# Kernel tuning notes

Measured on AMD Instinct MI355X. Metric: run time of the kernel, lower is better.

The kernel has to match this reference:

```python
import jax, jax.numpy as jnp
import numpy as np

# --- static configuration (matches init_kwargs / input_specs) ---
B, QB, D, NH, HD = 4, 512, 256, 8, 32   # batch, queries/batch, d_model, heads, head_dim
HALF = HD // 2                            # rotation pairs per head
L = 4                                     # n_levels
SIZES = [3, 5, 7, 9]                      # neighborhood size per level
K = sum(s * s for s in SIZES)             # 164 keys per query
SHAPES = np.array([[8, 8], [16, 16], [32, 32], [64, 64]], dtype=np.int32)
HMAX = 64                                 # finest-level spatial extent
LN_EPS = 1e-5
ROPE_THETA = 10.0


def make_rope_freqs():
    # Grouped-frequency ND RoPE: spatial dims (i, j) in freq group 0 (theta=10),
    # level dim in group 1 (theta = rope_theta/100 = 0.1). HALF slots split:
    # group0 -> HALF/2 (HALF/4 per spatial dim), group1 -> HALF/2.
    n_sp = HALF // 4   # 4 slots for i, 4 for j
    n_lv = HALF // 2   # 8 slots for level
    f = np.zeros((3, HALF), np.float32)
    f_sp = ROPE_THETA ** (-np.arange(n_sp, dtype=np.float32) / n_sp)
    f_lv = (ROPE_THETA / 100.0) ** (-np.arange(n_lv, dtype=np.float32) / n_lv)
    f[0, 0:n_sp] = f_sp
    f[1, n_sp:2 * n_sp] = f_sp
    f[2, 2 * n_sp:] = f_lv
    return jnp.asarray(np.tile(f[None], (NH, 1, 1)))  # [NH, 3, HALF]


def neighborhood_indices(qpos, shapes):
    # qpos: [N,4] float (b, i, j, level); queries live at the finest level so
    # (i, j) are full-scale coords. Returns (b,i,j,l) int indices [N,K,4] and
    # full-scale key positions (i_full, j_full, level) [N,K,3].
    N = qpos.shape[0]
    b = qpos[:, 0].astype(jnp.int32)
    q_ij = qpos[:, 1:3]
    shapes_f = shapes.astype(jnp.float32)
    scal = shapes_f / shapes_f[-1]  # [L,2]: H_l / H_finest
    idx_parts, pos_parts = [], []
    for m, size in enumerate(SIZES):
        center = jnp.floor(q_ij * scal[m]).astype(jnp.int32)  # [N,2] at level m
        r = jnp.arange(size, dtype=jnp.int32) - (size - 1) // 2
        off = jnp.stack(jnp.meshgrid(r, r, indexing='ij'), -1).reshape(-1, 2)
        nb = center[:, None, :] + off[None]                    # [N, s*s, 2]
        lev_i = jnp.full((N, size * size, 1), m, jnp.int32)
        idx_parts.append(jnp.concatenate([nb, lev_i], -1))
        pos_parts.append(jnp.concatenate(
            [nb.astype(jnp.float32) / scal[m],                 # back to full scale
             jnp.full((N, size * size, 1), float(m))], -1))
    ijl = jnp.concatenate(idx_parts, 1)       # [N,K,3]
    key_pos = jnp.concatenate(pos_parts, 1)   # [N,K,3]
    bijl = jnp.concatenate([jnp.broadcast_to(b[:, None, None], (N, K, 1)), ijl], -1)
    return bijl, key_pos


def gather_values(fmap, bijl, shapes):
    # fmap: dense stand-in for the sparse COO pyramid, [B, HMAX, HMAX, L, D];
    # level l only occupies the top-left [H_l, W_l] block -> out-of-range keys
    # are "unspecified" (value 0, masked out of the softmax).
    b, i, j, l = bijl[..., 0], bijl[..., 1], bijl[..., 2], bijl[..., 3]
    hw = shapes[l]  # [N,K,2]
    valid = (i >= 0) & (i < hw[..., 0]) & (j >= 0) & (j < hw[..., 1])
    ic = jnp.clip(i, 0, HMAX - 1)
    jc = jnp.clip(j, 0, HMAX - 1)
    val = fmap[b, ic, jc, l]  # [N,K,D]
    return val * valid[..., None], valid


def layer_norm(x, g, b_):
    mu = x.mean(-1, keepdims=True)
    var = ((x - mu) ** 2).mean(-1, keepdims=True)
    return (x - mu) * jax.lax.rsqrt(var + LN_EPS) * g + b_


def apply_rope(x, pos, freqs):
    # x: [..., NH, HD], pos: [..., 3], freqs: [NH, 3, HALF]
    ang = jnp.einsum('...p,hpf->...hf', pos, freqs)
    c, s = jnp.cos(ang), jnp.sin(ang)
    xr = x.reshape(x.shape[:-1] + (HALF, 2))
    x1, x2 = xr[..., 0], xr[..., 1]
    return jnp.stack([x1 * c - x2 * s, x1 * s + x2 * c], -1).reshape(x.shape)


def setup_inputs() -> dict:
    key = jax.random.key(0)
    ks = jax.random.split(key, 8)
    N = B * QB
    q_ij = jax.random.uniform(ks[0], (N, 2), minval=0.5, maxval=float(HMAX) - 0.5)
    batch = jnp.repeat(jnp.arange(B, dtype=jnp.float32), QB)
    lev = jnp.full((N, 1), float(L - 1))  # all queries at the finest level
    query_positions_bijl = jnp.concatenate([batch[:, None], q_ij, lev], -1)
    sc = D ** -0.5
    return {
        'query': jax.random.normal(ks[1], (N, D), jnp.float32),
        'query_positions_bijl': query_positions_bijl,
        'query_batch_offsets': jnp.arange(B + 1, dtype=jnp.int32) * QB,
        'stacked_feature_maps': jax.random.normal(ks[2], (B, HMAX, HMAX, L, D), jnp.float32),
        'level_spatial_shapes': jnp.asarray(SHAPES),
        'ln_gamma': jnp.ones((D,), jnp.float32),
        'ln_beta': jnp.zeros((D,), jnp.float32),
        'Wq': jax.random.normal(ks[3], (D, D), jnp.float32) * sc,
        'Wkv': jax.random.normal(ks[4], (D, 2 * D), jnp.float32) * sc,
        'Wout': jax.random.normal(ks[5], (D, D), jnp.float32) * sc,
        'rope_freqs': make_rope_freqs(),
    }


def reference(query, query_positions_bijl, query_batch_offsets, stacked_feature_maps,
              level_spatial_shapes, ln_gamma, ln_beta, Wq, Wkv, Wout, rope_freqs):
    N = query.shape[0]
    bijl, key_pos = neighborhood_indices(query_positions_bijl, level_spatial_shapes)
    value, specified = gather_values(stacked_feature_maps, bijl, level_spatial_shapes)
    residual = query
    qn = layer_norm(query, ln_gamma, ln_beta)  # norm_first
    q = qn @ Wq                                # [N, D]
    kv = value @ Wkv                           # [N, K, 2D]
    k, v = jnp.split(kv, 2, axis=-1)
    q = apply_rope(q.reshape(B, QB, NH, HD),
                   query_positions_bijl[:, 1:].reshape(B, QB, 3), rope_freqs)
    k = apply_rope(k.reshape(B, QB, K, NH, HD),
                   key_pos.reshape(B, QB, K, 3), rope_freqs)
    v = v.reshape(B, QB, K, NH, HD)
    # NOTE: original module applies no 1/sqrt(head_dim) scaling -- kept faithful.
    scores = jnp.einsum('bqhd,bqkhd->bhqk', q, k)
    mask = specified.reshape(B, QB, K)[:, None]  # [B,1,QB,K]
    scores = jnp.where(mask, scores, -jnp.inf)
    w = jax.nn.softmax(scores, axis=-1)
    x = jnp.einsum('bhqk,bqkhd->bqhd', w, v)
    x = x.reshape(N, D) @ Wout
    return x + residual
```

## Files before the change

### kernel.cpp

```cpp
#include <hip/hip_runtime.h>
#include <math.h>

#define NQ    2048
#define Dd    256
#define NHh   8
#define HDd   32
#define KK    164
#define KP    192
#define PPB   5440
#define M_TOT 21760
#define TWO_D 512

using bf16x8  = __attribute__((ext_vector_type(8))) short;
using f32x4   = __attribute__((ext_vector_type(4))) float;
using ushort8 = __attribute__((ext_vector_type(8))) unsigned short;

__device__ __forceinline__ unsigned short bf16_rne(float x) {
    unsigned u = __float_as_uint(x);
    return (unsigned short)((u + 0x7fffu + ((u >> 16) & 1u)) >> 16);
}
__device__ __forceinline__ float bf2f(unsigned short h) {
    return __uint_as_float((unsigned)h << 16);
}

__device__ __forceinline__ void gload_lds16(const void* g, void* s) {
    __builtin_amdgcn_global_load_lds(
        (const __attribute__((address_space(1))) void*)g,
        (__attribute__((address_space(3))) void*)s, 16, 0, 0);
}

__device__ __forceinline__ void row_geom(int r, int& l, int& S, int& base, int& lg, int& inv) {
    if      (r < 64)   { l = 0; S = 8;  base = 0;    lg = 3; inv = 8; }
    else if (r < 320)  { l = 1; S = 16; base = 64;   lg = 4; inv = 4; }
    else if (r < 1344) { l = 2; S = 32; base = 320;  lg = 5; inv = 2; }
    else               { l = 3; S = 64; base = 1344; lg = 6; inv = 1; }
}

__global__ __launch_bounds__(256) void gather_split(const float* __restrict__ fmap,
                                                    unsigned short* __restrict__ Ahi,
                                                    unsigned short* __restrict__ Alo) {
    int gid = blockIdx.x * 256 + threadIdx.x;
    int m = gid >> 6, c4 = (gid & 63) << 2;
    int b = m / PPB, r = m - b * PPB;
    int l, S, base, lg, inv;
    row_geom(r, l, S, base, lg, inv);
    int idx = r - base;
    int i = idx >> lg, j = idx & (S - 1);
    size_t rowOff = ((size_t)((b * 64 + i) * 64 + j)) * 1024 + l * 256;
    const float4 v = *(const float4*)(fmap + rowOff + c4);
    ushort4 hi, lo;
    hi.x = bf16_rne(v.x); lo.x = bf16_rne(v.x - __uint_as_float((unsigned)hi.x << 16));
    hi.y = bf16_rne(v.y); lo.y = bf16_rne(v.y - __uint_as_float((unsigned)hi.y << 16));
    hi.z = bf16_rne(v.z); lo.z = bf16_rne(v.z - __uint_as_float((unsigned)hi.z << 16));
    hi.w = bf16_rne(v.w); lo.w = bf16_rne(v.w - __uint_as_float((unsigned)hi.w << 16));
    *(ushort4*)(Ahi + (size_t)m * 256 + c4) = hi;
    *(ushort4*)(Alo + (size_t)m * 256 + c4) = lo;
}

__global__ __launch_bounds__(256) void splitw_t(const float* __restrict__ W,
                                                unsigned short* __restrict__ Bthi,
                                                unsigned short* __restrict__ Btlo,
                                                int N) {
    int gid = blockIdx.x * 256 + threadIdx.x;
    int k = gid & 255, n = gid >> 8;
    float x = W[k * N + n];
    unsigned short h = bf16_rne(x);
    unsigned short lo = bf16_rne(x - __uint_as_float((unsigned)h << 16));
    Bthi[n * 256 + k] = h;
    Btlo[n * 256 + k] = lo;
}

__global__ __launch_bounds__(256) void kv_gemm_mfma(const unsigned short* __restrict__ Ahi,
                                                    const unsigned short* __restrict__ Alo,
                                                    const unsigned short* __restrict__ Bthi,
                                                    const unsigned short* __restrict__ Btlo,
                                                    unsigned short* __restrict__ kv16) {
    __shared__ __align__(16) short As[2][128 * 32];
    __shared__ __align__(16) short Bs[2][128 * 32];

    const int t  = threadIdx.x;
    const int w  = t >> 6, l = t & 63;
    const int wr = w >> 1, wc = w & 1;
    const int bm = blockIdx.x * 128, n0 = blockIdx.y * 128;
    const int lr = l & 15, ks = l >> 4;
    const int ksw8 = ((ks ^ ((lr >> 1) & 3)) << 3);

    f32x4 acc[4][4];
#pragma unroll
    for (int i = 0; i < 4; i++)
#pragma unroll
        for (int j = 0; j < 4; j++) { f32x4 z = {0.f,0.f,0.f,0.f}; acc[i][j] = z; }

    const int srow = l >> 2, sslot = l & 3;
    const int gs = sslot ^ ((srow >> 1) & 3);

    auto stage = [&](int kt, int buf) {
        int seg = kt >> 3;
        const unsigned short* Aseg = (seg < 2) ? Ahi : Alo;
        const unsigned short* Bseg = (seg == 1) ? Btlo : Bthi;
        size_t k0b = (size_t)((kt & 7) << 6);
#pragma unroll
        for (int i = 0; i < 2; i++) {
            int rb = w * 32 + i * 16;
            int m  = rb + srow;
            gload_lds16((const char*)Aseg + (((size_t)(bm + m)) << 9) + k0b + (gs << 4),
                        (void*)&As[buf][rb * 32]);
            gload_lds16((const char*)Bseg + (((size_t)(n0 + m)) << 9) + k0b + (gs << 4),
                        (void*)&Bs[buf][rb * 32]);
        }
    };

    stage(0, 0);
    __syncthreads();

    for (int kt = 0; kt < 24; kt++) {
        int cur = kt & 1;
        if (kt < 23) stage(kt + 1, cur ^ 1);

        bf16x8 afr[4], bfr[4];
#pragma unroll
        for (int f = 0; f < 4; f++) {
            int m = wr * 64 + f * 16 + lr;
            afr[f] = *(const bf16x8*)&As[cur][m * 32 + ksw8];
            int n = wc * 64 + f * 16 + lr;
            bfr[f] = *(const bf16x8*)&Bs[cur][n * 32 + ksw8];
        }
#pragma unroll
        for (int i = 0; i < 4; i++)
#pragma unroll
            for (int j = 0; j < 4; j++)
                acc[i][j] = __builtin_amdgcn_mfma_f32_16x16x32_bf16(afr[i], bfr[j],
                                                                    acc[i][j], 0, 0, 0);
        __syncthreads();
    }

#pragma unroll
    for (int i = 0; i < 4; i++) {
        int mg = bm + wr * 64 + i * 16 + ks * 4;
#pragma unroll
        for (int j = 0; j < 4; j++) {
            int ng = n0 + wc * 64 + j * 16 + lr;
#pragma unroll
            for (int r = 0; r < 4; r++) {
                float self = acc[i][j][r];
                float part = __shfl_xor(self, 1);
                if (!(lr & 1)) {
                    unsigned word = (unsigned)bf16_rne(self)
                                  | ((unsigned)bf16_rne(part) << 16);
                    *(unsigned*)(kv16 + (size_t)(mg + r) * TWO_D + ng) = word;
                }
            }
        }
    }
}

template<bool RESID>
__global__ __launch_bounds__(256) void proj_gemm(const unsigned short* __restrict__ Ahi,
                                                 const unsigned short* __restrict__ Alo,
                                                 const unsigned short* __restrict__ Bthi,
                                                 const unsigned short* __restrict__ Btlo,
                                                 float* __restrict__ C,
                                                 const float* __restrict__ resid) {
    __shared__ __align__(16) short As[2][128 * 32];
    __shared__ __align__(16) short Bs[2][64 * 32];

    const int t  = threadIdx.x;
    const int w  = t >> 6, l = t & 63;
    const int bm = blockIdx.x * 128, n0 = blockIdx.y * 64;
    const int lr = l & 15, ks = l >> 4;
    const int ksw8 = ((ks ^ ((lr >> 1) & 3)) << 3);

    f32x4 acc[2][4];
#pragma unroll
    for (int i = 0; i < 2; i++)
#pragma unroll
        for (int j = 0; j < 4; j++) { f32x4 z = {0.f,0.f,0.f,0.f}; acc[i][j] = z; }

    const int srow = l >> 2, sslot = l & 3;
    const int gs = sslot ^ ((srow >> 1) & 3);

    auto stage = [&](int kt, int buf) {
        int seg = kt >> 3;
        const unsigned short* Aseg = (seg < 2) ? Ahi : Alo;
        const unsigned short* Bseg = (seg == 1) ? Btlo : Bthi;
        size_t k0b = (size_t)((kt & 7) << 6);
#pragma unroll
        for (int i = 0; i < 2; i++) {
            int rb = w * 32 + i * 16;
            int m  = rb + srow;
            gload_lds16((const char*)Aseg + (((size_t)(bm + m)) << 9) + k0b + (gs << 4),
                        (void*)&As[buf][rb * 32]);
        }
        {
            int rb = w * 16;
            int m  = rb + srow;
            gload_lds16((const char*)Bseg + (((size_t)(n0 + m)) << 9) + k0b + (gs << 4),
                        (void*)&Bs[buf][rb * 32]);
        }
    };

    stage(0, 0);
    __syncthreads();

    for (int kt = 0; kt < 24; kt++) {
        int cur = kt & 1;
        if (kt < 23) stage(kt + 1, cur ^ 1);

        bf16x8 afr[2], bfr[4];
#pragma unroll
        for (int f = 0; f < 2; f++) {
            int m = w * 32 + f * 16 + lr;
            afr[f] = *(const bf16x8*)&As[cur][m * 32 + ksw8];
        }
#pragma unroll
        for (int j = 0; j < 4; j++) {
            int n = j * 16 + lr;
            bfr[j] = *(const bf16x8*)&Bs[cur][n * 32 + ksw8];
        }
#pragma unroll
        for (int i = 0; i < 2; i++)
#pragma unroll
            for (int j = 0; j < 4; j++)
                acc[i][j] = __builtin_amdgcn_mfma_f32_16x16x32_bf16(afr[i], bfr[j],
                                                                    acc[i][j], 0, 0, 0);
        __syncthreads();
    }

#pragma unroll
    for (int i = 0; i < 2; i++) {
        int mg = bm + w * 32 + i * 16 + ks * 4;
#pragma unroll
        for (int j = 0; j < 4; j++) {
            int ng = n0 + j * 16 + lr;
#pragma unroll
            for (int r = 0; r < 4; r++) {
                float v = acc[i][j][r];
                if (RESID) v += resid[(size_t)(mg + r) * 256 + ng];
                C[(size_t)(mg + r) * 256 + ng] = v;
            }
        }
    }
}

__global__ __launch_bounds__(256) void rope_k(unsigned short* __restrict__ kv16,
                                              const float* __restrict__ freqs) {
    int gid = blockIdx.x * 256 + threadIdx.x;
    int m = gid >> 7;
    int p = gid & 127;
    int f = p & 15;

    int b = m / PPB;
    int r = m - b * PPB;
    int l, S, base, lg, inv;
    row_geom(r, l, S, base, lg, inv);
    int idx = r - base;
    int i = idx >> lg;
    int j = idx & (S - 1);

    float px = (float)(i * inv), py = (float)(j * inv), pl = (float)l;
    float ang = px * freqs[f] + py * freqs[16 + f] + pl * freqs[32 + f];
    float c = cosf(ang), s = sinf(ang);

    unsigned* kp = (unsigned*)kv16 + (size_t)m * 256 + p;
    unsigned v = *kp;
    float x1 = bf2f((unsigned short)(v & 0xffff));
    float x2 = bf2f((unsigned short)(v >> 16));
    float y1 = x1 * c - x2 * s;
    float y2 = x1 * s + x2 * c;
    *kp = (unsigned)bf16_rne(y1) | ((unsigned)bf16_rne(y2) << 16);
}

__global__ __launch_bounds__(256) void ln_split(const float* __restrict__ query,
                                                const float* __restrict__ gamma,
                                                const float* __restrict__ beta,
                                                unsigned short* __restrict__ Xhi,
                                                unsigned short* __restrict__ Xlo) {
    __shared__ float red[4];
    const int q = blockIdx.x, t = threadIdx.x, wid = t >> 6;

    float x = query[q * Dd + t];
    float s = x;
#pragma unroll
    for (int mK = 32; mK >= 1; mK >>= 1) s += __shfl_xor(s, mK);
    if ((t & 63) == 0) red[wid] = s;
    __syncthreads();
    float mu = (red[0] + red[1] + red[2] + red[3]) * (1.0f / 256.0f);
    float dx = x - mu;
    float s2 = dx * dx;
#pragma unroll
    for (int mK = 32; mK >= 1; mK >>= 1) s2 += __shfl_xor(s2, mK);
    __syncthreads();
    if ((t & 63) == 0) red[wid] = s2;
    __syncthreads();
    float var = (red[0] + red[1] + red[2] + red[3]) * (1.0f / 256.0f);
    float v = dx * rsqrtf(var + 1e-5f) * gamma[t] + beta[t];
    unsigned short hi = bf16_rne(v);
    Xhi[q * Dd + t] = hi;
    Xlo[q * Dd + t] = bf16_rne(v - __uint_as_float((unsigned)hi << 16));
}

__global__ __launch_bounds__(256) void attn_core(const float* __restrict__ qr,
                                                 const float* __restrict__ qpos,
                                                 const unsigned short* __restrict__ kv16,
                                                 const float* __restrict__ freqs,
                                                 unsigned short* __restrict__ Phi,
                                                 unsigned short* __restrict__ Plo) {
    __shared__ __align__(16) float qsh[Dd];
    __shared__ float sL[NHh * KP];
    __shared__ int   kidx[KP];
    __shared__ float attnP[8][Dd];
    __shared__ float invS[NHh];

    const int q = ((blockIdx.x & 7) << 8) | (blockIdx.x >> 3);
    const int t = threadIdx.x;
    const int h = t >> 5, lane = t & 31;

    float qx = qpos[q * 4 + 1];
    float qy = qpos[q * 4 + 2];
    int   bb = (int)qpos[q * 4 + 0];

    {
        float x = qr[q * Dd + t];
        int f = (t & 31) >> 1;
        float ang = qx * freqs[f] + qy * freqs[16 + f] + 3.0f * freqs[32 + f];
        float c = cosf(ang), sn = sinf(ang);
        float partner = __shfl_xor(x, 1);
        qsh[t] = (!(t & 1)) ? (x * c - partner * sn) : (partner * sn + x * c);
    }

    if (t < KP) {
        int k = t;
        int kv = -1;
        if (k < KK) {
            int S, base, off, sz, half, lg;
            if      (k < 9)  { S = 8;  base = 0;    off = k;      sz = 3; half = 1; lg = 3; }
            else if (k < 34) { S = 16; base = 64;   off = k - 9;  sz = 5; half = 2; lg = 4; }
            else if (k < 83) { S = 32; base = 320;  off = k - 34; sz = 7; half = 3; lg = 5; }
            else             { S = 64; base = 1344; off = k - 83; sz = 9; half = 4; lg = 6; }
            int di = off / sz - half;
            int dj = off % sz - half;
            float scal = (float)S * (1.0f / 64.0f);
            int ci = (int)floorf(qx * scal);
            int cj = (int)floorf(qy * scal);
            int i = ci + di, j = cj + dj;
            bool valid = (i >= 0) & (i < S) & (j >= 0) & (j < S);
            kv = valid ? (bb * PPB + base + (i << lg) + j) : -1;
        }
        kidx[t] = kv;
    }
    __syncthreads();

    float qreg[32];
#pragma unroll
    for (int i = 0; i < 32; i++) qreg[i] = qsh[h * HDd + i];

#pragma unroll
    for (int ct = 0; ct < 6; ++ct) {
        int k = ct * 32 + lane;
        int ki = kidx[k];
        int kr = ki < 0 ? 0 : ki;
        const ushort8* kp = (const ushort8*)(kv16 + (size_t)kr * TWO_D + h * HDd);
        float c0 = 0.f, c1 = 0.f;
#pragma unroll
        for (int s4 = 0; s4 < 4; s4++) {
            ushort8 kvv = kp[s4];
            float* cc = (s4 & 1) ? &c1 : &c0;
#pragma unroll
            for (int e = 0; e < 8; e++)
                *cc = fmaf(qreg[s4 * 8 + e], bf2f(kvv[e]), *cc);
        }
        sL[h * KP + k] = (ki >= 0) ? (c0 + c1) : -INFINITY;
    }
    __syncthreads();

    float mx = -INFINITY;
#pragma unroll
    for (int ct = 0; ct < 6; ++ct) mx = fmaxf(mx, sL[h * KP + ct * 32 + lane]);
#pragma unroll
    for (int mK = 16; mK >= 1; mK >>= 1) mx = fmaxf(mx, __shfl_xor(mx, mK));
    float se = 0.f;
#pragma unroll
    for (int ct = 0; ct < 6; ++ct) {
        int k = ct * 32 + lane;
        float e = __expf(sL[h * KP + k] - mx);
        sL[h * KP + k] = e;
        se += e;
    }
#pragma unroll
    for (int mK = 16; mK >= 1; mK >>= 1) se += __shfl_xor(se, mK);
    if (lane == 0) invS[h] = 1.0f / se;
    __syncthreads();

    {
        const int rep  = t >> 6;
        const int half = (t >> 5) & 1;
        const int l5   = t & 31;
        const int hh   = l5 >> 2;
        const int oct  = l5 & 3;
        float a[8];
#pragma unroll
        for (int e = 0; e < 8; e++) a[e] = 0.f;
        const unsigned short* vbase = kv16 + Dd + hh * HDd + oct * 8;
#pragma unroll 4
        for (int it = 0; it < 24; it++) {
            int k = rep * 48 + it * 2 + half;
            float w0 = sL[hh * KP + k];
            int kr = kidx[k]; kr = kr < 0 ? 0 : kr;
            ushort8 vv = *(const ushort8*)(vbase + (size_t)kr * TWO_D);
#pragma unroll
            for (int e = 0; e < 8; e++) a[e] = fmaf(w0, bf2f(vv[e]), a[e]);
        }
        float* dst = &attnP[t >> 5][hh * HDd + oct * 8];
#pragma unroll
        for (int e = 0; e < 8; e++) dst[e] = a[e];
    }
    __syncthreads();

    float val = 0.f;
#pragma unroll
    for (int s = 0; s < 8; s++) val += attnP[s][t];
    val *= invS[h];
    unsigned short hi = bf16_rne(val);
    Phi[q * Dd + t] = hi;
    Plo[q * Dd + t] = bf16_rne(val - __uint_as_float((unsigned)hi << 16));
}

#define BMf 128
#define BNf 128
#define KTf 16

__global__ __launch_bounds__(256) void kv_gemm(const float* __restrict__ fmap,
                                               const float* __restrict__ Wkv,
                                               float* __restrict__ kvws) {
    __shared__ float Asf[KTf][BMf + 4];
    __shared__ float Bsf[KTf][BNf + 4];
    __shared__ int   rowOff[BMf];

    const int t  = threadIdx.x;
    const int bm = blockIdx.x * BMf;
    const int n0 = blockIdx.y * BNf;

    if (t < BMf) {
        int m = bm + t;
        int b = m / PPB;
        int r = m - b * PPB;
        int l, S, base, lg, inv;
        row_geom(r, l, S, base, lg, inv);
        int idx = r - base;
        int i = idx >> lg;
        int j = idx & (S - 1);
        rowOff[t] = ((b * 64 + i) * 64 + j) * 1024 + l * 256;
    }
    __syncthreads();

    const int tx = t & 15, ty = t >> 4;
    float acc[8][8];
#pragma unroll
    for (int i = 0; i < 8; i++)
#pragma unroll
        for (int j = 0; j < 8; j++) acc[i][j] = 0.f;

    for (int k0 = 0; k0 < Dd; k0 += KTf) {
#pragma unroll
        for (int s = 0; s < 2; s++) {
            int task = t + s * 256;
            int row  = task >> 2;
            int k4   = (task & 3) * 4;
            const float4 v = *(const float4*)(fmap + rowOff[row] + k0 + k4);
            Asf[k4 + 0][row] = v.x;
            Asf[k4 + 1][row] = v.y;
            Asf[k4 + 2][row] = v.z;
            Asf[k4 + 3][row] = v.w;
        }
#pragma unroll
        for (int s = 0; s < 2; s++) {
            int task = t + s * 256;
            int kk   = task >> 5;
            int c4   = (task & 31) * 4;
            *(float4*)(&Bsf[kk][c4]) = *(const float4*)(Wkv + (k0 + kk) * TWO_D + n0 + c4);
        }
        __syncthreads();
#pragma unroll
        for (int kk = 0; kk < KTf; kk++) {
            float a[8], bb[8];
#pragma unroll
            for (int i = 0; i < 8; i++) a[i]  = Asf[kk][ty * 8 + i];
#pragma unroll
            for (int j = 0; j < 8; j++) bb[j] = Bsf[kk][tx * 8 + j];
#pragma unroll
            for (int i = 0; i < 8; i++)
#pragma unroll
                for (int j = 0; j < 8; j++)
                    acc[i][j] = fmaf(a[i], bb[j], acc[i][j]);
        }
        __syncthreads();
    }

#pragma unroll
    for (int i = 0; i < 8; i++) {
        int m = bm + ty * 8 + i;
        float* dst = kvws + (size_t)m * TWO_D + n0 + tx * 8;
#pragma unroll
        for (int j = 0; j < 8; j += 4) {
            *(float4*)(dst + j) = make_float4(acc[i][j], acc[i][j + 1],
                                              acc[i][j + 2], acc[i][j + 3]);
        }
    }
}

__global__ __launch_bounds__(256) void rope_k_f32(float* __restrict__ kvws,
                                                  const float* __restrict__ freqs) {
    int gid = blockIdx.x * 256 + threadIdx.x;
    int m = gid >> 7;
    int p = gid & 127;
    int f = p & 15;
    int b = m / PPB;
    int r = m - b * PPB;
    int l, S, base, lg, inv;
    row_geom(r, l, S, base, lg, inv);
    int idx = r - base;
    int i = idx >> lg;
    int j = idx & (S - 1);
    float px = (float)(i * inv), py = (float)(j * inv), pl = (float)l;
    float ang = px * freqs[f] + py * freqs[16 + f] + pl * freqs[32 + f];
    float c = cosf(ang), s = sinf(ang);
    float2* kp = (float2*)kvws + (size_t)m * 256 + p;
    float2 v = *kp;
    *kp = make_float2(v.x * c - v.y * s, v.x * s + v.y * c);
}

__global__ __launch_bounds__(256) void attn_fused(const float* __restrict__ query,
                                                  const float* __restrict__ qpos,
                                                  const float* __restrict__ Wq,
                                                  const float* __restrict__ Wout,
                                                  const float* __restrict__ gamma,
                                                  const float* __restrict__ beta,
                                                  const float* __restrict__ freqs,
                                                  const float* __restrict__ kvws,
                                                  float* __restrict__ out) {
    __shared__ float qn[Dd];
    __shared__ __align__(16) float qsh[Dd];
    __shared__ float sL[NHh * KK];
    __shared__ int   kidx[KK];
    __shared__ float attnL[Dd];
    __shared__ float red[4];
    __shared__ float invS[NHh];

    const int q = blockIdx.x;
    const int t = threadIdx.x;
    const int wid = t >> 6;
    const int h = t >> 5, lane = t & 31;

    float x = query[q * Dd + t];
    float s = x;
#pragma unroll
    for (int mK = 32; mK >= 1; mK >>= 1) s += __shfl_xor(s, mK);
    if ((t & 63) == 0) red[wid] = s;
    __syncthreads();
    float mu = (red[0] + red[1] + red[2] + red[3]) * (1.0f / 256.0f);
    float dx = x - mu;
    float s2 = dx * dx;
#pragma unroll
    for (int mK = 32; mK >= 1; mK >>= 1) s2 += __shfl_xor(s2, mK);
    __syncthreads();
    if ((t & 63) == 0) red[wid] = s2;
    __syncthreads();
    float var = (red[0] + red[1] + red[2] + red[3]) * (1.0f / 256.0f);
    float rs = rsqrtf(var + 1e-5f);
    qn[t] = dx * rs * gamma[t] + beta[t];
    __syncthreads();

    float a0 = 0.f, a1 = 0.f, a2 = 0.f, a3 = 0.f;
#pragma unroll 8
    for (int d = 0; d < Dd; d += 4) {
        a0 = fmaf(qn[d + 0], Wq[(d + 0) * Dd + t], a0);
        a1 = fmaf(qn[d + 1], Wq[(d + 1) * Dd + t], a1);
        a2 = fmaf(qn[d + 2], Wq[(d + 2) * Dd + t], a2);
        a3 = fmaf(qn[d + 3], Wq[(d + 3) * Dd + t], a3);
    }
    float acc = (a0 + a1) + (a2 + a3);

    float qx = qpos[q * 4 + 1];
    float qy = qpos[q * 4 + 2];
    int   bb = (int)qpos[q * 4 + 0];
    {
        int f = (t & 31) >> 1;
        float ang = qx * freqs[f] + qy * freqs[16 + f] + 3.0f * freqs[32 + f];
        float c = cosf(ang), sn = sinf(ang);
        float partner = __shfl_xor(acc, 1);
        bool ev = !(t & 1);
        acc = ev ? (acc * c - partner * sn) : (partner * sn + acc * c);
    }
    qsh[t] = acc;

    if (t < KK) {
        int k = t;
        int S, base, off, sz, half, lg;
        if      (k < 9)  { S = 8;  base = 0;    off = k;      sz = 3; half = 1; lg = 3; }
        else if (k < 34) { S = 16; base = 64;   off = k - 9;  sz = 5; half = 2; lg = 4; }
        else if (k < 83) { S = 32; base = 320;  off = k - 34; sz = 7; half = 3; lg = 5; }
        else             { S = 64; base = 1344; off = k - 83; sz = 9; half = 4; lg = 6; }
        int di = off / sz - half;
        int dj = off % sz - half;
        float scal = (float)S * (1.0f / 64.0f);
        int ci = (int)floorf(qx * scal);
        int cj = (int)floorf(qy * scal);
        int i = ci + di, j = cj + dj;
        bool valid = (i >= 0) & (i < S) & (j >= 0) & (j < S);
        kidx[t] = valid ? (bb * PPB + base + (i << lg) + j) : -1;
    }
    __syncthreads();

    float4 qv[8];
    {
        const float4* qp = (const float4*)(qsh + h * HDd);
#pragma unroll
        for (int i = 0; i < 8; i++) qv[i] = qp[i];
    }
#pragma unroll
    for (int ct = 0; ct < 6; ++ct) {
        int k = ct * 32 + lane;
        if (k >= KK) break;
        int ki = kidx[k];
        int kr = ki < 0 ? 0 : ki;
        const float4* kp = (const float4*)(kvws + (size_t)kr * TWO_D + h * HDd);
        float c0 = 0.f, c1 = 0.f;
#pragma unroll
        for (int i = 0; i < 8; i += 2) {
            float4 k0v = kp[i], k1v = kp[i + 1];
            c0 = fmaf(qv[i].x, k0v.x, c0); c0 = fmaf(qv[i].y, k0v.y, c0);
            c0 = fmaf(qv[i].z, k0v.z, c0); c0 = fmaf(qv[i].w, k0v.w, c0);
            c1 = fmaf(qv[i + 1].x, k1v.x, c1); c1 = fmaf(qv[i + 1].y, k1v.y, c1);
            c1 = fmaf(qv[i + 1].z, k1v.z, c1); c1 = fmaf(qv[i + 1].w, k1v.w, c1);
        }
        sL[h * KK + k] = (ki >= 0) ? (c0 + c1) : -INFINITY;
    }
    __syncthreads();

    float mx = -INFINITY;
    for (int k = lane; k < KK; k += 32) mx = fmaxf(mx, sL[h * KK + k]);
#pragma unroll
    for (int mK = 16; mK >= 1; mK >>= 1) mx = fmaxf(mx, __shfl_xor(mx, mK));
    float se = 0.f;
    for (int k = lane; k < KK; k += 32) {
        float e = expf(sL[h * KK + k] - mx);
        sL[h * KK + k] = e;
        se += e;
    }
#pragma unroll
    for (int mK = 16; mK >= 1; mK >>= 1) se += __shfl_xor(se, mK);
    if (lane == 0) invS[h] = 1.0f / se;
    __syncthreads();

    float p0 = 0.f, p1 = 0.f, p2 = 0.f, p3 = 0.f;
#pragma unroll 4
    for (int k = 0; k < 164; k += 4) {
        int ki0 = kidx[k],     kr0 = ki0 < 0 ? 0 : ki0;
        int ki1 = kidx[k + 1], kr1 = ki1 < 0 ? 0 : ki1;
        int ki2 = kidx[k + 2], kr2 = ki2 < 0 ? 0 : ki2;
        int ki3 = kidx[k + 3], kr3 = ki3 < 0 ? 0 : ki3;
        p0 = fmaf(sL[h * KK + k],     kvws[(size_t)kr0 * TWO_D + Dd + t], p0);
        p1 = fmaf(sL[h * KK + k + 1], kvws[(size_t)kr1 * TWO_D + Dd + t], p1);
        p2 = fmaf(sL[h * KK + k + 2], kvws[(size_t)kr2 * TWO_D + Dd + t], p2);
        p3 = fmaf(sL[h * KK + k + 3], kvws[(size_t)kr3 * TWO_D + Dd + t], p3);
    }
    attnL[t] = ((p0 + p1) + (p2 + p3)) * invS[h];
    __syncthreads();

    float o0 = query[q * Dd + t], o1 = 0.f, o2 = 0.f, o3 = 0.f;
#pragma unroll 8
    for (int d = 0; d < Dd; d += 4) {
        o0 = fmaf(attnL[d + 0], Wout[(d + 0) * Dd + t], o0);
        o1 = fmaf(attnL[d + 1], Wout[(d + 1) * Dd + t], o1);
        o2 = fmaf(attnL[d + 2], Wout[(d + 2) * Dd + t], o2);
        o3 = fmaf(attnL[d + 3], Wout[(d + 3) * Dd + t], o3);
    }
    out[q * Dd + t] = (o0 + o1) + (o2 + o3);
}

extern "C" void kernel_launch(void* const* d_in, const int* in_sizes, int n_in,
                              void* d_out, int out_size, void* d_ws, size_t ws_size,
                              hipStream_t stream) {
    const float* query = (const float*)d_in[0];
    const float* qpos  = (const float*)d_in[1];
    const float* fmap  = (const float*)d_in[3];
    const float* gamma = (const float*)d_in[5];
    const float* beta  = (const float*)d_in[6];
    const float* Wq    = (const float*)d_in[7];
    const float* Wkv   = (const float*)d_in[8];
    const float* Wout  = (const float*)d_in[9];
    const float* freqs = (const float*)d_in[10];
    float* out = (float*)d_out;

    const size_t KV_B = (size_t)M_TOT * TWO_D * 4;
    const size_t A_B  = (size_t)M_TOT * Dd * 2;
    const size_t WT_B = (size_t)Dd * TWO_D * 2;
    const size_t need = KV_B + 2 * A_B + 2 * WT_B;

    if (ws_size >= need) {
        char* base = (char*)d_ws;
        unsigned short* kv16   = (unsigned short*)base;
        unsigned short* Ahi    = (unsigned short*)(base + KV_B);
        unsigned short* Alo    = (unsigned short*)(base + KV_B + A_B);
        unsigned short* WkvThi = (unsigned short*)(base + KV_B + 2 * A_B);
        unsigned short* WkvTlo = (unsigned short*)(base + KV_B + 2 * A_B + WT_B);
        unsigned short* Phi    = (unsigned short*)(base + KV_B);
        unsigned short* Plo    = (unsigned short*)(base + KV_B + 1048576);
        float*          qrw    = (float*)        (base + KV_B + 2097152);
        unsigned short* WqThi  = (unsigned short*)(base + KV_B + 4194304);
        unsigned short* WqTlo  = (unsigned short*)(base + KV_B + 4325376);
        unsigned short* WoThi  = (unsigned short*)(base + KV_B + 4456448);
        unsigned short* WoTlo  = (unsigned short*)(base + KV_B + 4587520);

        gather_split<<<dim3((M_TOT * 64) / 256), 256, 0, stream>>>(fmap, Ahi, Alo);
        splitw_t<<<dim3(512), 256, 0, stream>>>(Wkv, WkvThi, WkvTlo, 512);
        kv_gemm_mfma<<<dim3(M_TOT / 128, 4), 256, 0, stream>>>(Ahi, Alo, WkvThi, WkvTlo, kv16);
        rope_k<<<dim3((M_TOT * 128) / 256), 256, 0, stream>>>(kv16, freqs);
        ln_split<<<dim3(NQ), 256, 0, stream>>>(query, gamma, beta, Phi, Plo);
        splitw_t<<<dim3(256), 256, 0, stream>>>(Wq, WqThi, WqTlo, 256);
        splitw_t<<<dim3(256), 256, 0, stream>>>(Wout, WoThi, WoTlo, 256);
        proj_gemm<false><<<dim3(NQ / 128, 4), 256, 0, stream>>>(Phi, Plo, WqThi, WqTlo,
                                                                qrw, nullptr);
        attn_core<<<dim3(NQ), 256, 0, stream>>>(qrw, qpos, kv16, freqs, Phi, Plo);
        proj_gemm<true><<<dim3(NQ / 128, 4), 256, 0, stream>>>(Phi, Plo, WoThi, WoTlo,
                                                               out, query);
    } else {
        float* kvws = (float*)d_ws;
        kv_gemm<<<dim3(M_TOT / BMf, TWO_D / BNf), 256, 0, stream>>>(fmap, Wkv, kvws);
        rope_k_f32<<<dim3((M_TOT * 128) / 256), 256, 0, stream>>>(kvws, freqs);
        attn_fused<<<dim3(NQ), 256, 0, stream>>>(query, qpos, Wq, Wout, gamma, beta,
                                                 freqs, kvws, out);
    }
}
```

Measured before the change: 223.0 us.

## Fuse prep kernels, fold RoPE into KV GEMM epilogue, shrink projection tiles

Merges the gather/split, the three weight-split kernels and the LayerNorm split into one prep launch. The separate K RoPE pass moves into the KV GEMM epilogue, so kv16 is no longer read and rewritten. The grid axes are swapped so column tiles of the same row block run adjacently. The projection GEMMs move to 64x32 tiles, giving more blocks for better occupancy on the small N=2048 problem. This cuts launch overhead and one full pass over the KV buffer, at the cost of extra trig work and branching in the GEMM epilogue.

```diff
diff --git a/kernel.cpp b/kernel.cpp
--- a/kernel.cpp
+++ b/kernel.cpp
@@ -36,44 +36,89 @@
     else               { l = 3; S = 64; base = 1344; lg = 6; inv = 1; }
 }
 
-__global__ __launch_bounds__(256) void gather_split(const float* __restrict__ fmap,
-                                                    unsigned short* __restrict__ Ahi,
-                                                    unsigned short* __restrict__ Alo) {
-    int gid = blockIdx.x * 256 + threadIdx.x;
-    int m = gid >> 6, c4 = (gid & 63) << 2;
-    int b = m / PPB, r = m - b * PPB;
-    int l, S, base, lg, inv;
-    row_geom(r, l, S, base, lg, inv);
-    int idx = r - base;
-    int i = idx >> lg, j = idx & (S - 1);
-    size_t rowOff = ((size_t)((b * 64 + i) * 64 + j)) * 1024 + l * 256;
-    const float4 v = *(const float4*)(fmap + rowOff + c4);
-    ushort4 hi, lo;
-    hi.x = bf16_rne(v.x); lo.x = bf16_rne(v.x - __uint_as_float((unsigned)hi.x << 16));
-    hi.y = bf16_rne(v.y); lo.y = bf16_rne(v.y - __uint_as_float((unsigned)hi.y << 16));
-    hi.z = bf16_rne(v.z); lo.z = bf16_rne(v.z - __uint_as_float((unsigned)hi.z << 16));
-    hi.w = bf16_rne(v.w); lo.w = bf16_rne(v.w - __uint_as_float((unsigned)hi.w << 16));
-    *(ushort4*)(Ahi + (size_t)m * 256 + c4) = hi;
-    *(ushort4*)(Alo + (size_t)m * 256 + c4) = lo;
-}
-
-__global__ __launch_bounds__(256) void splitw_t(const float* __restrict__ W,
-                                                unsigned short* __restrict__ Bthi,
-                                                unsigned short* __restrict__ Btlo,
-                                                int N) {
-    int gid = blockIdx.x * 256 + threadIdx.x;
+__device__ __forceinline__ void split_one(const float* __restrict__ W,
+                                          unsigned short* __restrict__ hi_,
+                                          unsigned short* __restrict__ lo_,
+                                          int N, int gid) {
     int k = gid & 255, n = gid >> 8;
     float x = W[k * N + n];
     unsigned short h = bf16_rne(x);
-    unsigned short lo = bf16_rne(x - __uint_as_float((unsigned)h << 16));
-    Bthi[n * 256 + k] = h;
-    Btlo[n * 256 + k] = lo;
+    hi_[n * 256 + k] = h;
+    lo_[n * 256 + k] = bf16_rne(x - bf2f(h));
+}
+
+__global__ __launch_bounds__(256) void prep(const float* __restrict__ fmap,
+                                            const float* __restrict__ Wkv,
+                                            const float* __restrict__ Wq,
+                                            const float* __restrict__ Wout,
+                                            const float* __restrict__ query,
+                                            const float* __restrict__ gamma,
+                                            const float* __restrict__ beta,
+                                            unsigned short* __restrict__ Ahi,
+                                            unsigned short* __restrict__ Alo,
+                                            unsigned short* __restrict__ WkvThi,
+                                            unsigned short* __restrict__ WkvTlo,
+                                            unsigned short* __restrict__ WqThi,
+                                            unsigned short* __restrict__ WqTlo,
+                                            unsigned short* __restrict__ WoThi,
+                                            unsigned short* __restrict__ WoTlo,
+                                            unsigned short* __restrict__ Xhi,
+                                            unsigned short* __restrict__ Xlo) {
+    __shared__ float red[4];
+    const int bid = blockIdx.x, t = threadIdx.x;
+
+    if (bid < 5440) {
+        int gid = bid * 256 + t;
+        int m = gid >> 6, c4 = (gid & 63) << 2;
+        int b = m / PPB, r = m - b * PPB;
+        int l, S, base, lg, inv;
+        row_geom(r, l, S, base, lg, inv);
+        int idx = r - base;
+        int i = idx >> lg, j = idx & (S - 1);
+        size_t rowOff = ((size_t)((b * 64 + i) * 64 + j)) * 1024 + l * 256;
+        const float4 v = *(const float4*)(fmap + rowOff + c4);
+        ushort4 hi, lo;
+        hi.x = bf16_rne(v.x); lo.x = bf16_rne(v.x - bf2f(hi.x));
+        hi.y = bf16_rne(v.y); lo.y = bf16_rne(v.y - bf2f(hi.y));
+        hi.z = bf16_rne(v.z); lo.z = bf16_rne(v.z - bf2f(hi.z));
+        hi.w = bf16_rne(v.w); lo.w = bf16_rne(v.w - bf2f(hi.w));
+        *(ushort4*)(Ahi + (size_t)m * 256 + c4) = hi;
+        *(ushort4*)(Alo + (size_t)m * 256 + c4) = lo;
+    } else if (bid < 5952) {
+        split_one(Wkv, WkvThi, WkvTlo, 512, (bid - 5440) * 256 + t);
+    } else if (bid < 6208) {
+        split_one(Wq, WqThi, WqTlo, 256, (bid - 5952) * 256 + t);
+    } else if (bid < 6464) {
+        split_one(Wout, WoThi, WoTlo, 256, (bid - 6208) * 256 + t);
+    } else {
+        const int q = bid - 6464, wid = t >> 6;
+        float x = query[q * Dd + t];
+        float s = x;
+#pragma unroll
+        for (int mK = 32; mK >= 1; mK >>= 1) s += __shfl_xor(s, mK);
+        if ((t & 63) == 0) red[wid] = s;
+        __syncthreads();
+        float mu = (red[0] + red[1] + red[2] + red[3]) * (1.0f / 256.0f);
+        float dx = x - mu;
+        float s2 = dx * dx;
+#pragma unroll
+        for (int mK = 32; mK >= 1; mK >>= 1) s2 += __shfl_xor(s2, mK);
+        __syncthreads();
+        if ((t & 63) == 0) red[wid] = s2;
+        __syncthreads();
+        float var = (red[0] + red[1] + red[2] + red[3]) * (1.0f / 256.0f);
+        float v = dx * rsqrtf(var + 1e-5f) * gamma[t] + beta[t];
+        unsigned short hi = bf16_rne(v);
+        Xhi[q * Dd + t] = hi;
+        Xlo[q * Dd + t] = bf16_rne(v - bf2f(hi));
+    }
 }
 
 __global__ __launch_bounds__(256) void kv_gemm_mfma(const unsigned short* __restrict__ Ahi,
                                                     const unsigned short* __restrict__ Alo,
                                                     const unsigned short* __restrict__ Bthi,
                                                     const unsigned short* __restrict__ Btlo,
+                                                    const float* __restrict__ freqs,
                                                     unsigned short* __restrict__ kv16) {
     __shared__ __align__(16) short As[2][128 * 32];
     __shared__ __align__(16) short Bs[2][128 * 32];
@@ -81,9 +126,10 @@
     const int t  = threadIdx.x;
     const int w  = t >> 6, l = t & 63;
     const int wr = w >> 1, wc = w & 1;
-    const int bm = blockIdx.x * 128, n0 = blockIdx.y * 128;
+    const int n0 = blockIdx.x * 128, bm = blockIdx.y * 128;
     const int lr = l & 15, ks = l >> 4;
     const int ksw8 = ((ks ^ ((lr >> 1) & 3)) << 3);
+    const bool doRope = (n0 < 256);
 
     f32x4 acc[4][4];
 #pragma unroll
@@ -138,16 +184,35 @@
     for (int i = 0; i < 4; i++) {
         int mg = bm + wr * 64 + i * 16 + ks * 4;
 #pragma unroll
-        for (int j = 0; j < 4; j++) {
-            int ng = n0 + wc * 64 + j * 16 + lr;
-#pragma unroll
-            for (int r = 0; r < 4; r++) {
+        for (int r = 0; r < 4; r++) {
+            int m = mg + r;
+            float px = 0.f, py = 0.f, pl = 0.f;
+            if (doRope) {
+                int b = m / PPB;
+                int rr = m - b * PPB;
+                int lL, S, base, lg, inv;
+                row_geom(rr, lL, S, base, lg, inv);
+                int idx = rr - base;
+                px = (float)((idx >> lg) * inv);
+                py = (float)((idx & (S - 1)) * inv);
+                pl = (float)lL;
+            }
+#pragma unroll
+            for (int j = 0; j < 4; j++) {
+                int ng = n0 + wc * 64 + j * 16 + lr;
                 float self = acc[i][j][r];
                 float part = __shfl_xor(self, 1);
                 if (!(lr & 1)) {
-                    unsigned word = (unsigned)bf16_rne(self)
-                                  | ((unsigned)bf16_rne(part) << 16);
-                    *(unsigned*)(kv16 + (size_t)(mg + r) * TWO_D + ng) = word;
+                    float y1 = self, y2 = part;
+                    if (doRope) {
+                        int f = (ng & 31) >> 1;
+                        float ang = px * freqs[f] + py * freqs[16 + f] + pl * freqs[32 + f];
+                        float c = cosf(ang), s = sinf(ang);
+                        y1 = self * c - part * s;
+                        y2 = self * s + part * c;
+                    }
+                    unsigned word = (unsigned)bf16_rne(y1) | ((unsigned)bf16_rne(y2) << 16);
+                    *(unsigned*)(kv16 + (size_t)m * TWO_D + ng) = word;
                 }
             }
         }
@@ -161,20 +226,18 @@
                                                  const unsigned short* __restrict__ Btlo,
                                                  float* __restrict__ C,
                                                  const float* __restrict__ resid) {
-    __shared__ __align__(16) short As[2][128 * 32];
-    __shared__ __align__(16) short Bs[2][64 * 32];
+    __shared__ __align__(16) short As[2][64 * 32];
+    __shared__ __align__(16) short Bs[2][32 * 32];
 
     const int t  = threadIdx.x;
     const int w  = t >> 6, l = t & 63;
-    const int bm = blockIdx.x * 128, n0 = blockIdx.y * 64;
+    const int n0 = blockIdx.x * 32, bm = blockIdx.y * 64;
     const int lr = l & 15, ks = l >> 4;
     const int ksw8 = ((ks ^ ((lr >> 1) & 3)) << 3);
 
-    f32x4 acc[2][4];
-#pragma unroll
-    for (int i = 0; i < 2; i++)
-#pragma unroll
-        for (int j = 0; j < 4; j++) { f32x4 z = {0.f,0.f,0.f,0.f}; acc[i][j] = z; }
+    f32x4 acc[2];
+#pragma unroll
+    for (int j = 0; j < 2; j++) { f32x4 z = {0.f,0.f,0.f,0.f}; acc[j] = z; }
 
     const int srow = l >> 2, sslot = l & 3;
     const int gs = sslot ^ ((srow >> 1) & 3);
@@ -184,14 +247,13 @@
         const unsigned short* Aseg = (seg < 2) ? Ahi : Alo;
         const unsigned short* Bseg = (seg == 1) ? Btlo : Bthi;
         size_t k0b = (size_t)((kt & 7) << 6);
-#pragma unroll
-        for (int i = 0; i < 2; i++) {
-            int rb = w * 32 + i * 16;
+        {
+            int rb = w * 16;
             int m  = rb + srow;
             gload_lds16((const char*)Aseg + (((size_t)(bm + m)) << 9) + k0b + (gs << 4),
                         (void*)&As[buf][rb * 32]);
         }
-        {
+        if (w < 2) {
             int rb = w * 16;
             int m  = rb + srow;
             gload_lds16((const char*)Bseg + (((size_t)(n0 + m)) << 9) + k0b + (gs << 4),
@@ -206,97 +268,35 @@
         int cur = kt & 1;
         if (kt < 23) stage(kt + 1, cur ^ 1);
 
-        bf16x8 afr[2], bfr[4];
-#pragma unroll
-        for (int f = 0; f < 2; f++) {
-            int m = w * 32 + f * 16 + lr;
-            afr[f] = *(const bf16x8*)&As[cur][m * 32 + ksw8];
-        }
-#pragma unroll
-        for (int j = 0; j < 4; j++) {
+        bf16x8 afr, bfr[2];
+        {
+            int m = w * 16 + lr;
+            afr = *(const bf16x8*)&As[cur][m * 32 + ksw8];
+        }
+#pragma unroll
+        for (int j = 0; j < 2; j++) {
             int n = j * 16 + lr;
             bfr[j] = *(const bf16x8*)&Bs[cur][n * 32 + ksw8];
         }
 #pragma unroll
-        for (int i = 0; i < 2; i++)
-#pragma unroll
-            for (int j = 0; j < 4; j++)
-                acc[i][j] = __builtin_amdgcn_mfma_f32_16x16x32_bf16(afr[i], bfr[j],
-                                                                    acc[i][j], 0, 0, 0);
+        for (int j = 0; j < 2; j++)
+            acc[j] = __builtin_amdgcn_mfma_f32_16x16x32_bf16(afr, bfr[j], acc[j], 0, 0, 0);
         __syncthreads();
     }
 
-#pragma unroll
-    for (int i = 0; i < 2; i++) {
-        int mg = bm + w * 32 + i * 16 + ks * 4;
-#pragma unroll
-        for (int j = 0; j < 4; j++) {
+    {
+        int mg = bm + w * 16 + ks * 4;
+#pragma unroll
+        for (int j = 0; j < 2; j++) {
             int ng = n0 + j * 16 + lr;
 #pragma unroll
             for (int r = 0; r < 4; r++) {
-                float v = acc[i][j][r];
+                float v = acc[j][r];
                 if (RESID) v += resid[(size_t)(mg + r) * 256 + ng];
                 C[(size_t)(mg + r) * 256 + ng] = v;
             }
         }
     }
-}
-
-__global__ __launch_bounds__(256) void rope_k(unsigned short* __restrict__ kv16,
-                                              const float* __restrict__ freqs) {
-    int gid = blockIdx.x * 256 + threadIdx.x;
-    int m = gid >> 7;
-    int p = gid & 127;
-    int f = p & 15;
-
-    int b = m / PPB;
-    int r = m - b * PPB;
-    int l, S, base, lg, inv;
-    row_geom(r, l, S, base, lg, inv);
-    int idx = r - base;
-    int i = idx >> lg;
-    int j = idx & (S - 1);
-
-    float px = (float)(i * inv), py = (float)(j * inv), pl = (float)l;
-    float ang = px * freqs[f] + py * freqs[16 + f] + pl * freqs[32 + f];
-    float c = cosf(ang), s = sinf(ang);
-
-    unsigned* kp = (unsigned*)kv16 + (size_t)m * 256 + p;
-    unsigned v = *kp;
-    float x1 = bf2f((unsigned short)(v & 0xffff));
-    float x2 = bf2f((unsigned short)(v >> 16));
-    float y1 = x1 * c - x2 * s;
-    float y2 = x1 * s + x2 * c;
-    *kp = (unsigned)bf16_rne(y1) | ((unsigned)bf16_rne(y2) << 16);
-}
-
-__global__ __launch_bounds__(256) void ln_split(const float* __restrict__ query,
-                                                const float* __restrict__ gamma,
-                                                const float* __restrict__ beta,
-                                                unsigned short* __restrict__ Xhi,
-                                                unsigned short* __restrict__ Xlo) {
-    __shared__ float red[4];
-    const int q = blockIdx.x, t = threadIdx.x, wid = t >> 6;
-
-    float x = query[q * Dd + t];
-    float s = x;
-#pragma unroll
-    for (int mK = 32; mK >= 1; mK >>= 1) s += __shfl_xor(s, mK);
-    if ((t & 63) == 0) red[wid] = s;
-    __syncthreads();
-    float mu = (red[0] + red[1] + red[2] + red[3]) * (1.0f / 256.0f);
-    float dx = x - mu;
-    float s2 = dx * dx;
-#pragma unroll
-    for (int mK = 32; mK >= 1; mK >>= 1) s2 += __shfl_xor(s2, mK);
-    __syncthreads();
-    if ((t & 63) == 0) red[wid] = s2;
-    __syncthreads();
-    float var = (red[0] + red[1] + red[2] + red[3]) * (1.0f / 256.0f);
-    float v = dx * rsqrtf(var + 1e-5f) * gamma[t] + beta[t];
-    unsigned short hi = bf16_rne(v);
-    Xhi[q * Dd + t] = hi;
-    Xlo[q * Dd + t] = bf16_rne(v - __uint_as_float((unsigned)hi << 16));
 }
 
 __global__ __launch_bounds__(256) void attn_core(const float* __restrict__ qr,
@@ -422,7 +422,7 @@
     val *= invS[h];
     unsigned short hi = bf16_rne(val);
     Phi[q * Dd + t] = hi;
-    Plo[q * Dd + t] = bf16_rne(val - __uint_as_float((unsigned)hi << 16));
+    Plo[q * Dd + t] = bf16_rne(val - bf2f(hi));
 }
 
 #define BMf 128
@@ -692,38 +692,49 @@
     const float* freqs = (const float*)d_in[10];
     float* out = (float*)d_out;
 
-    const size_t KV_B = (size_t)M_TOT * TWO_D * 4;
-    const size_t A_B  = (size_t)M_TOT * Dd * 2;
-    const size_t WT_B = (size_t)Dd * TWO_D * 2;
-    const size_t need = KV_B + 2 * A_B + 2 * WT_B;
+    const size_t O_KV16   = 0;
+    const size_t O_AHI    = 22282240;
+    const size_t O_ALO    = 33423360;
+    const size_t O_WKVHI  = 44564480;
+    const size_t O_WKVLO  = 44826624;
+    const size_t O_WQHI   = 45088768;
+    const size_t O_WQLO   = 45219840;
+    const size_t O_WOHI   = 45350912;
+    const size_t O_WOLO   = 45481984;
+    const size_t O_XHI    = 45613056;
+    const size_t O_XLO    = 46661632;
+    const size_t O_QR     = 47710208;
+    const size_t O_PHI    = 49807360;
+    const size_t O_PLO    = 50855936;
+    const size_t need     = 51904512;
 
     if (ws_size >= need) {
         char* base = (char*)d_ws;
-        unsigned short* kv16   = (unsigned short*)base;
-        unsigned short* Ahi    = (unsigned short*)(base + KV_B);
-        unsigned short* Alo    = (unsigned short*)(base + KV_B + A_B);
-        unsigned short* WkvThi = (unsigned short*)(base + KV_B + 2 * A_B);
-        unsigned short* WkvTlo = (unsigned short*)(base + KV_B + 2 * A_B + WT_B);
-        unsigned short* Phi    = (unsigned short*)(base + KV_B);
-        unsigned short* Plo    = (unsigned short*)(base + KV_B + 1048576);
-        float*          qrw    = (float*)        (base + KV_B + 2097152);
-        unsigned short* WqThi  = (unsigned short*)(base + KV_B + 4194304);
-        unsigned short* WqTlo  = (unsigned short*)(base + KV_B + 4325376);
-        unsigned short* WoThi  = (unsigned short*)(base + KV_B + 4456448);
-        unsigned short* WoTlo  = (unsigned short*)(base + KV_B + 4587520);
-
-        gather_split<<<dim3((M_TOT * 64) / 256), 256, 0, stream>>>(fmap, Ahi, Alo);
-        splitw_t<<<dim3(512), 256, 0, stream>>>(Wkv, WkvThi, WkvTlo, 512);
-        kv_gemm_mfma<<<dim3(M_TOT / 128, 4), 256, 0, stream>>>(Ahi, Alo, WkvThi, WkvTlo, kv16);
-        rope_k<<<dim3((M_TOT * 128) / 256), 256, 0, stream>>>(kv16, freqs);
-        ln_split<<<dim3(NQ), 256, 0, stream>>>(query, gamma, beta, Phi, Plo);
-        splitw_t<<<dim3(256), 256, 0, stream>>>(Wq, WqThi, WqTlo, 256);
-        splitw_t<<<dim3(256), 256, 0, stream>>>(Wout, WoThi, WoTlo, 256);
-        proj_gemm<false><<<dim3(NQ / 128, 4), 256, 0, stream>>>(Phi, Plo, WqThi, WqTlo,
-                                                                qrw, nullptr);
+        unsigned short* kv16   = (unsigned short*)(base + O_KV16);
+        unsigned short* Ahi    = (unsigned short*)(base + O_AHI);
+        unsigned short* Alo    = (unsigned short*)(base + O_ALO);
+        unsigned short* WkvThi = (unsigned short*)(base + O_WKVHI);
+        unsigned short* WkvTlo = (unsigned short*)(base + O_WKVLO);
+        unsigned short* WqThi  = (unsigned short*)(base + O_WQHI);
+        unsigned short* WqTlo  = (unsigned short*)(base + O_WQLO);
+        unsigned short* WoThi  = (unsigned short*)(base + O_WOHI);
+        unsigned short* WoTlo  = (unsigned short*)(base + O_WOLO);
+        unsigned short* Xhi    = (unsigned short*)(base + O_XHI);
+        unsigned short* Xlo    = (unsigned short*)(base + O_XLO);
+        float*          qrw    = (float*)        (base + O_QR);
+        unsigned short* Phi    = (unsigned short*)(base + O_PHI);
+        unsigned short* Plo    = (unsigned short*)(base + O_PLO);
+
+        prep<<<dim3(8512), 256, 0, stream>>>(fmap, Wkv, Wq, Wout, query, gamma, beta,
+                                             Ahi, Alo, WkvThi, WkvTlo,
+                                             WqThi, WqTlo, WoThi, WoTlo, Xhi, Xlo);
+        kv_gemm_mfma<<<dim3(4, 170), 256, 0, stream>>>(Ahi, Alo, WkvThi, WkvTlo,
+                                                       freqs, kv16);
+        proj_gemm<false><<<dim3(8, 32), 256, 0, stream>>>(Xhi, Xlo, WqThi, WqTlo,
+                                                          qrw, nullptr);
         attn_core<<<dim3(NQ), 256, 0, stream>>>(qrw, qpos, kv16, freqs, Phi, Plo);
-        proj_gemm<true><<<dim3(NQ / 128, 4), 256, 0, stream>>>(Phi, Plo, WoThi, WoTlo,
-                                                               out, query);
+        proj_gemm<true><<<dim3(8, 32), 256, 0, stream>>>(Phi, Plo, WoThi, WoTlo,
+                                                         out, query);
     } else {
         float* kvws = (float*)d_ws;
         kv_gemm<<<dim3(M_TOT / BMf, TWO_D / BNf), 256, 0, stream>>>(fmap, Wkv, kvws);
```

After: 284.0 us. 27.4% more time.
